# Kernel tuning notes

Measured on AMD Instinct MI355X. Metric: run time of the kernel, lower is better.

## Reference

```python
import jax, jax.numpy as jnp
import numpy as np

B, S, D_IN, D_H, D_OUT = 4, 2048, 512, 512, 512


def setup_inputs() -> dict:
    key = jax.random.key(0)
    ks = jax.random.split(key, 11)
    s_in = 1.0 / np.sqrt(D_IN)
    s_cat = 1.0 / np.sqrt(3 * D_H)
    return {
        "x1": jax.random.normal(ks[0], (B, S, D_IN), jnp.float32),
        "x2": jax.random.normal(ks[1], (B, S, D_IN), jnp.float32),
        "x3": jax.random.normal(ks[2], (B, S, D_IN), jnp.float32),
        "Wq": jax.random.normal(ks[3], (D_IN, D_H), jnp.float32) * s_in,
        "bq": jnp.zeros((D_H,), jnp.float32),
        "Wk": jax.random.normal(ks[4], (D_IN, D_H), jnp.float32) * s_in,
        "bk": jnp.zeros((D_H,), jnp.float32),
        "Wv": jax.random.normal(ks[5], (D_IN, D_H), jnp.float32) * s_in,
        "bv": jnp.zeros((D_H,), jnp.float32),
        "Wo": jax.random.normal(ks[6], (3 * D_H, D_OUT), jnp.float32) * s_cat,
        "bo": jnp.zeros((D_OUT,), jnp.float32),
    }


def _attn(Q, K, V):
    # Q: [B,S,H], K/V: [B,S,H] -> [B,S,H]
    scale = 1.0 / jnp.sqrt(jnp.asarray(K.shape[-1], Q.dtype))
    scores = jnp.einsum('bqh,bkh->bqk', Q, K) * scale
    w = jax.nn.softmax(scores, axis=-1)
    return jnp.einsum('bqk,bkh->bqh', w, V)


def reference(x1, x2, x3, Wq, bq, Wk, bk, Wv, bv, Wo, bo):
    Q1, Q2, Q3 = x1 @ Wq + bq, x2 @ Wq + bq, x3 @ Wq + bq
    K1, K2, K3 = x1 @ Wk + bk, x2 @ Wk + bk, x3 @ Wk + bk
    V1, V2, V3 = x1 @ Wv + bv, x2 @ Wv + bv, x3 @ Wv + bv
    fused_x1 = _attn(Q1, K2, V2) + _attn(Q1, K3, V3)
    fused_x2 = _attn(Q2, K1, V1) + _attn(Q2, K3, V3)
    fused_x3 = _attn(Q3, K1, V1) + _attn(Q3, K2, V2)
    fused = jnp.concatenate([fused_x1, fused_x2, fused_x3], axis=-1)
    return fused @ Wo + bo
```

## Files before the change

kernel.cpp:

```cpp
#include <hip/hip_runtime.h>
#include <hip/hip_bf16.h>

typedef __attribute__((ext_vector_type(4))) float  f32x4;
typedef __attribute__((ext_vector_type(8))) short  short8;

#define GAS(p) ((const __attribute__((address_space(1))) void*)(p))
#define LAS(p) ((__attribute__((address_space(3))) void*)(p))

__device__ inline short bf16_of(float f) {
    union { float f; unsigned u; } v; v.f = f;
    unsigned r = v.u + 0x7FFFu + ((v.u >> 16) & 1u);
    return (short)(r >> 16);
}

#define MFMA __builtin_amdgcn_mfma_f32_16x16x32_bf16

__device__ __forceinline__ void stage64(const short* A, long lda,
                                        const short* B, long ldb,
                                        short* As, short* Bs) {
    const int tid = threadIdx.x;
    const int w = tid >> 6, l = tid & 63;
    const int r = l >> 3;
    const int scol = ((l & 7) ^ r) * 8;
#pragma unroll
    for (int q = 0; q < 4; ++q) {
        const int rowb = q * 32 + w * 8;
        __builtin_amdgcn_global_load_lds(GAS(A + (long)(rowb + r) * lda + scol),
                                         LAS(As + rowb * 64), 16, 0, 0);
        __builtin_amdgcn_global_load_lds(GAS(B + (long)(rowb + r) * ldb + scol),
                                         LAS(Bs + rowb * 64), 16, 0, 0);
    }
}

__device__ __forceinline__ void gemm_core64(const short* A, long lda,
                                            const short* B, long ldb, int nk,
                                            short* sA, short* sB,
                                            f32x4 acc[4][4]) {
    const int tid = threadIdx.x;
    const int lane = tid & 63, wid = tid >> 6;
    const int wr = wid >> 1, wc = wid & 1;
    const int fr = lane & 15, fk = lane >> 4;
    const int swz = (fr & 7) << 4;
    const int abase = (wr * 64 + fr) * 128 + fk * 16;
    const int bbase = (wc * 64 + fr) * 128 + fk * 16;

    stage64(A, lda, B, ldb, sA, sB);
    __syncthreads();
    for (int ks = 0; ks < nk; ++ks) {
        const int cur = ks & 1;
        if (ks + 1 < nk)
            stage64(A + (ks + 1) * 64, lda, B + (ks + 1) * 64, ldb,
                    sA + (cur ^ 1) * 8192, sB + (cur ^ 1) * 8192);
        const char* pa = (const char*)(sA + cur * 8192);
        const char* pb = (const char*)(sB + cur * 8192);
        short8 af[2][4], bfr[2][4];
#pragma unroll
        for (int kk = 0; kk < 2; ++kk) {
#pragma unroll
            for (int mi = 0; mi < 4; ++mi)
                af[kk][mi] = *(const short8*)(pa + (((abase + kk * 64) ^ swz) + mi * 2048));
#pragma unroll
            for (int ni = 0; ni < 4; ++ni)
                bfr[kk][ni] = *(const short8*)(pb + (((bbase + kk * 64) ^ swz) + ni * 2048));
        }
#pragma unroll
        for (int kk = 0; kk < 2; ++kk)
#pragma unroll
            for (int mi = 0; mi < 4; ++mi)
#pragma unroll
                for (int ni = 0; ni < 4; ++ni)
                    acc[mi][ni] = MFMA(af[kk][mi], bfr[kk][ni], acc[mi][ni], 0, 0, 0);
        __syncthreads();
    }
}

__device__ __forceinline__ void bounce_store(short* Pb, const short vals[4][4][4],
                                             short* C, long ldc) {
    const int tid = threadIdx.x, lane = tid & 63, wid = tid >> 6;
    const int wr = wid >> 1, wc = wid & 1, fr = lane & 15, fk = lane >> 4;
#pragma unroll
    for (int mi = 0; mi < 4; ++mi)
#pragma unroll
        for (int ni = 0; ni < 4; ++ni)
#pragma unroll
            for (int r = 0; r < 4; ++r) {
                const int row = wr * 64 + mi * 16 + fk * 4 + r;
                const int col = wc * 64 + ni * 16 + fr;
                Pb[row * 128 + (col ^ ((row & 7) << 3))] = vals[mi][ni][r];
            }
    __syncthreads();
#pragma unroll
    for (int i = 0; i < 8; ++i) {
        const int row = i * 16 + (tid >> 4);
        const int ch = tid & 15;
        short8 v = *(const short8*)&Pb[row * 128 + ((ch * 8) ^ ((row & 7) << 3))];
        *(short8*)&C[(long)row * ldc + ch * 8] = v;
    }
}

__global__ __launch_bounds__(256, 2)
void proj_qk_k(const short* __restrict__ xb, const short* __restrict__ WqkT,
               short* __restrict__ Qb, short* __restrict__ Kb,
               const float* __restrict__ bq, const float* __restrict__ bk) {
    __shared__ short sA[2 * 8192], sB[2 * 8192];
    const short* Ab = xb + (long)blockIdx.x * 128 * 512;
    const short* Bb = WqkT + (long)blockIdx.y * 128 * 512;
    f32x4 acc[4][4] = {};
    gemm_core64(Ab, 512, Bb, 512, 8, sA, sB, acc);

    const int lane = threadIdx.x & 63, wid = threadIdx.x >> 6;
    const int wc = wid & 1, fr = lane & 15;
    const int qc0 = blockIdx.y * 128;
    const float* bias = qc0 < 512 ? bq + qc0 : bk + (qc0 - 512);
    short vals[4][4][4];
#pragma unroll
    for (int mi = 0; mi < 4; ++mi)
#pragma unroll
        for (int ni = 0; ni < 4; ++ni) {
            const float bv_ = bias[wc * 64 + ni * 16 + fr];
#pragma unroll
            for (int r = 0; r < 4; ++r)
                vals[mi][ni][r] = bf16_of(acc[mi][ni][r] + bv_);
        }
    short* dst = (qc0 < 512 ? Qb + qc0 : Kb + (qc0 - 512)) + (long)blockIdx.x * 128 * 512;
    bounce_store(sA, vals, dst, 512);
}

__global__ __launch_bounds__(256, 2)
void proj_vt_k(const short* __restrict__ WvT, const short* __restrict__ xb,
               short* __restrict__ VT, const float* __restrict__ bv) {
    __shared__ short sA[2 * 8192], sB[2 * 8192];
    const short* Ab = WvT + (long)blockIdx.x * 128 * 512;
    const short* Bb = xb + (long)blockIdx.y * 128 * 512;
    f32x4 acc[4][4] = {};
    gemm_core64(Ab, 512, Bb, 512, 8, sA, sB, acc);

    const int lane = threadIdx.x & 63, wid = threadIdx.x >> 6;
    const int wr = wid >> 1, fk = lane >> 4;
    short vals[4][4][4];
#pragma unroll
    for (int mi = 0; mi < 4; ++mi)
#pragma unroll
        for (int ni = 0; ni < 4; ++ni)
#pragma unroll
            for (int r = 0; r < 4; ++r) {
                const int rowg = blockIdx.x * 128 + wr * 64 + mi * 16 + fk * 4 + r;
                vals[mi][ni][r] = bf16_of(acc[mi][ni][r] + bv[rowg]);
            }
    bounce_store(sA, vals, VT + (long)blockIdx.x * 128 * 24576 + blockIdx.y * 128, 24576);
}

struct Off6 { long a[6], b[6]; };

__global__ __launch_bounds__(256, 2)
void qk_exp(const short* __restrict__ Qb, const short* __restrict__ Kb,
            short* __restrict__ Sc, float* __restrict__ lpart,
            Off6 o, int z0, int zmask, int zshift, float kscale) {
    __shared__ short sA[2 * 8192], sB[2 * 8192];
    const int bid = blockIdx.x;
    const int z = bid & zmask;
    const int t = bid >> zshift;
    const int bx = t & 15, by = t >> 4;
    const int slice = z0 + z;
    const int gp = slice >> 2, b = slice & 3;
    const short* Ab = Qb + o.a[gp] + ((long)b * 2048 + (long)bx * 128) * 512;
    const short* Bb = Kb + o.b[gp] + ((long)b * 2048 + (long)by * 128) * 512;
    f32x4 acc[4][4] = {};
    gemm_core64(Ab, 512, Bb, 512, 8, sA, sB, acc);

    const int tid = threadIdx.x, lane = tid & 63, wid = tid >> 6;
    const int wr = wid >> 1, wc = wid & 1, fr = lane & 15, fk = lane >> 4;

#pragma unroll
    for (int mi = 0; mi < 4; ++mi)
#pragma unroll
        for (int ni = 0; ni < 4; ++ni)
#pragma unroll
            for (int r = 0; r < 4; ++r)
                acc[mi][ni][r] = exp2f(acc[mi][ni][r] * kscale);

#pragma unroll
    for (int mi = 0; mi < 4; ++mi)
#pragma unroll
        for (int r = 0; r < 4; ++r) {
            float s = acc[mi][0][r] + acc[mi][1][r] + acc[mi][2][r] + acc[mi][3][r];
            s += __shfl_xor(s, 1); s += __shfl_xor(s, 2);
            s += __shfl_xor(s, 4); s += __shfl_xor(s, 8);
            if (fr == 0)
                lpart[((long)z * 32 + by * 2 + wc) * 2048 +
                      (long)bx * 128 + wr * 64 + mi * 16 + fk * 4 + r] = s;
        }

    short vals[4][4][4];
#pragma unroll
    for (int mi = 0; mi < 4; ++mi)
#pragma unroll
        for (int ni = 0; ni < 4; ++ni)
#pragma unroll
            for (int r = 0; r < 4; ++r)
                vals[mi][ni][r] = bf16_of(acc[mi][ni][r]);

    short* Cb = Sc + (long)z * 2048 * 2048 +
                (long)bx * 128 * 2048 + (long)by * 128;
    bounce_store(sA, vals, Cb, 2048);
}

struct POff { long v[6], c[6]; };

__global__ __launch_bounds__(256, 2)
void pv_div(const short* __restrict__ Sc, const short* __restrict__ VT,
            const float* __restrict__ lpart, short* __restrict__ F,
            POff o, int z0, int zmask, int zshift) {
    __shared__ short sA[2 * 8192], sB[2 * 8192];
    const int bid = blockIdx.x;
    const int z = bid & zmask;
    const int t = bid >> zshift;
    const int bx = t & 15, by = t >> 4;
    const int slice = z0 + z;
    const int gp = slice >> 2, b = slice & 3;
    const short* Ab = Sc + (long)z * 2048 * 2048 + (long)bx * 128 * 2048;
    const short* Bb = VT + o.v[gp] + (long)b * 2048 + (long)by * 128 * 24576;
    f32x4 acc[4][4] = {};
    gemm_core64(Ab, 2048, Bb, 24576, 32, sA, sB, acc);

    const int tid = threadIdx.x, lane = tid & 63, wid = tid >> 6;
    const int wr = wid >> 1, wc = wid & 1, fr = lane & 15, fk = lane >> 4;

    float* linv_s = (float*)sB;
    if (tid < 128) {
        const float* lp = lpart + ((long)z * 32) * 2048 + (long)bx * 128 + tid;
        float s = 0.f;
#pragma unroll
        for (int j = 0; j < 32; ++j) s += lp[(long)j * 2048];
        linv_s[tid] = 1.0f / s;
    }
    __syncthreads();

    short vals[4][4][4];
#pragma unroll
    for (int mi = 0; mi < 4; ++mi) {
        float linv[4];
#pragma unroll
        for (int r = 0; r < 4; ++r) linv[r] = linv_s[wr * 64 + mi * 16 + fk * 4 + r];
#pragma unroll
        for (int ni = 0; ni < 4; ++ni)
#pragma unroll
            for (int r = 0; r < 4; ++r)
                vals[mi][ni][r] = bf16_of(acc[mi][ni][r] * linv[r]);
    }
    __syncthreads();

    short* Cb = F + ((long)b * 2048 + (long)bx * 128) * 3072 +
                o.c[gp] + (long)by * 128;
    bounce_store(sA, vals, Cb, 3072);
}

__device__ __forceinline__ void stage_f(const short* A, const short* B,
                                        short* As, short* Bs) {
    const int tid = threadIdx.x, w = tid >> 6, l = tid & 63;
    const int r = l >> 3, scol = ((l & 7) ^ r) * 8;
#pragma unroll
    for (int q = 0; q < 4; ++q) {
        const int rowb = q * 32 + w * 8;
        __builtin_amdgcn_global_load_lds(GAS(A + (long)(rowb + r) * 3072 + scol),
                                         LAS(As + rowb * 64), 16, 0, 0);
    }
#pragma unroll
    for (int q = 0; q < 2; ++q) {
        const int rowb = q * 32 + w * 8;
        __builtin_amdgcn_global_load_lds(GAS(B + (long)(rowb + r) * 3072 + scol),
                                         LAS(Bs + rowb * 64), 16, 0, 0);
    }
}

__global__ __launch_bounds__(256, 3)
void final64(const short* __restrict__ A, const short* __restrict__ B,
             float* __restrict__ C, const float* __restrict__ bias) {
    __shared__ short sA[2 * 8192], sB[2 * 4096];
    const short* Ab = A + (long)blockIdx.x * 128 * 3072;
    const short* Bb = B + (long)blockIdx.y * 64 * 3072;
    const int tid = threadIdx.x, lane = tid & 63, w = tid >> 6;
    const int fr = lane & 15, fk = lane >> 4;
    const int swz = (fr & 7) << 4;
    const int abase = (w * 32 + fr) * 128 + fk * 16;
    const int bbase = fr * 128 + fk * 16;

    f32x4 acc[2][4] = {};
    stage_f(Ab, Bb, sA, sB);
    __syncthreads();
    for (int ks = 0; ks < 48; ++ks) {
        const int cur = ks & 1;
        if (ks + 1 < 48)
            stage_f(Ab + (ks + 1) * 64, Bb + (ks + 1) * 64,
                    sA + (cur ^ 1) * 8192, sB + (cur ^ 1) * 4096);
        const char* pa = (const char*)(sA + cur * 8192);
        const char* pb = (const char*)(sB + cur * 4096);
        short8 af[2][2], bf[2][4];
#pragma unroll
        for (int kk = 0; kk < 2; ++kk) {
#pragma unroll
            for (int mi = 0; mi < 2; ++mi)
                af[kk][mi] = *(const short8*)(pa + (((abase + kk * 64) ^ swz) + mi * 2048));
#pragma unroll
            for (int ni = 0; ni < 4; ++ni)
                bf[kk][ni] = *(const short8*)(pb + (((bbase + kk * 64) ^ swz) + ni * 2048));
        }
#pragma unroll
        for (int kk = 0; kk < 2; ++kk)
#pragma unroll
            for (int mi = 0; mi < 2; ++mi)
#pragma unroll
                for (int ni = 0; ni < 4; ++ni)
                    acc[mi][ni] = MFMA(af[kk][mi], bf[kk][ni], acc[mi][ni], 0, 0, 0);
        __syncthreads();
    }
    const long r0 = (long)blockIdx.x * 128 + w * 32 + fk * 4;
    const long c0 = (long)blockIdx.y * 64 + fr;
#pragma unroll
    for (int mi = 0; mi < 2; ++mi)
#pragma unroll
        for (int ni = 0; ni < 4; ++ni) {
            const long rr = r0 + mi * 16, cc = c0 + ni * 16;
#pragma unroll
            for (int r = 0; r < 4; ++r)
                C[(rr + r) * 512 + cc] = acc[mi][ni][r] + bias[cc];
        }
}

__global__ __launch_bounds__(256)
void xconv(const float* __restrict__ x0, const float* __restrict__ x1,
           const float* __restrict__ x2, short* __restrict__ xb) {
    const float* s = blockIdx.z == 0 ? x0 : (blockIdx.z == 1 ? x1 : x2);
    const long i = ((long)blockIdx.x * 256 + threadIdx.x) * 8;
    f32x4 a = *(const f32x4*)(s + i), c = *(const f32x4*)(s + i + 4);
    short8 v;
    v[0] = bf16_of(a.x); v[1] = bf16_of(a.y); v[2] = bf16_of(a.z); v[3] = bf16_of(a.w);
    v[4] = bf16_of(c.x); v[5] = bf16_of(c.y); v[6] = bf16_of(c.z); v[7] = bf16_of(c.w);
    *(short8*)(xb + (long)blockIdx.z * 8192 * 512 + i) = v;
}

__global__ __launch_bounds__(256)
void wprep(const float* __restrict__ Wq, const float* __restrict__ Wk,
           const float* __restrict__ Wv, const float* __restrict__ Wo,
           short* __restrict__ WqkT, short* __restrict__ WvT,
           short* __restrict__ WoT2) {
    __shared__ float t[32][33];
    const int z = blockIdx.z;
    const float* src; short* dst; int rows; long ldd; bool dup = false;
    if (z == 0)      { src = Wq; dst = WqkT;              rows = 512;  ldd = 512; }
    else if (z == 1) { src = Wk; dst = WqkT + 512L * 512; rows = 512;  ldd = 512; }
    else if (z == 2) { src = Wv; dst = WvT;               rows = 512;  ldd = 512; }
    else             { src = Wo; dst = WoT2;              rows = 1536; ldd = 3072; dup = true; }
    const int r0 = blockIdx.x * 32, c0 = blockIdx.y * 32;
    if (r0 >= rows) return;
    const int lx = threadIdx.x & 31, ly = threadIdx.x >> 5;
#pragma unroll
    for (int p = 0; p < 4; ++p)
        t[ly + 8 * p][lx] = src[(long)(r0 + ly + 8 * p) * 512 + (c0 + lx)];
    __syncthreads();
#pragma unroll
    for (int p = 0; p < 4; ++p) {
        const short v = bf16_of(t[lx][ly + 8 * p]);
        const long base = (long)(c0 + ly + 8 * p) * ldd + (r0 + lx);
        dst[base] = v;
        if (dup) dst[base + 1536] = v;
    }
}

extern "C" void kernel_launch(void* const* d_in, const int* in_sizes, int n_in,
                              void* d_out, int out_size, void* d_ws, size_t ws_size,
                              hipStream_t stream) {
    const float* x[3] = { (const float*)d_in[0], (const float*)d_in[1], (const float*)d_in[2] };
    const float* Wq = (const float*)d_in[3]; const float* bq = (const float*)d_in[4];
    const float* Wk = (const float*)d_in[5]; const float* bk = (const float*)d_in[6];
    const float* Wv = (const float*)d_in[7]; const float* bv = (const float*)d_in[8];
    const float* Wo = (const float*)d_in[9]; const float* bo = (const float*)d_in[10];

    const long TOK = 8192, T3 = 3 * TOK;

    char* ws = (char*)d_ws;
    size_t off = 0;
    auto alloc = [&](size_t bytes) -> void* {
        void* pp = ws + off;
        off += (bytes + 255) & ~(size_t)255;
        return pp;
    };

    short* WqkT  = (short*)alloc(1024L * 512 * 2);
    short* WvT   = (short*)alloc(512L * 512 * 2);
    short* WoT2  = (short*)alloc(512L * 3072 * 2);
    short* Qb    = (short*)alloc(T3 * 512 * 2);
    short* Kb    = (short*)alloc(T3 * 512 * 2);
    short* VT    = (short*)alloc(512L * T3 * 2);
    short* fused = (short*)alloc(TOK * 3072 * 2);
    float* lpart = (float*)alloc(8L * 32 * 2048 * 4);
    short* xb    = (short*)alloc(T3 * 512 * 2);

    const size_t SLICE = 2048L * 2048 * 2;
    const size_t rem = ws_size > off ? ws_size - off : 0;
    const int nsl = (rem >= 8 * SLICE) ? 8 : 4;
    const int zshift = (nsl == 8) ? 3 : 2;
    short* scores = (short*)alloc((size_t)nsl * SLICE);

    const dim3 tb(256);
    wprep<<<dim3(48, 16, 4), tb, 0, stream>>>(Wq, Wk, Wv, Wo, WqkT, WvT, WoT2);
    xconv<<<dim3(2048, 1, 3), tb, 0, stream>>>(x[0], x[1], x[2], xb);

    proj_qk_k<<<dim3(192, 8), tb, 0, stream>>>(xb, WqkT, Qb, Kb, bq, bk);
    proj_vt_k<<<dim3(4, 192), tb, 0, stream>>>(WvT, xb, VT, bv);

    const int imap[6] = {0, 1, 2, 0, 1, 2};
    const int jmap[6] = {1, 0, 0, 2, 2, 1};
    Off6 qo{}; POff po{};
    for (int gp = 0; gp < 6; ++gp) {
        qo.a[gp] = (long)imap[gp] * TOK * 512;
        qo.b[gp] = (long)jmap[gp] * TOK * 512;
        po.v[gp] = (long)jmap[gp] * TOK;
        po.c[gp] = (long)imap[gp] * 512 + (gp >= 3 ? 1536 : 0);
    }
    const float kscale = 0.04419417382415922f * 1.4426950408889634f;

    for (int z0 = 0; z0 < 24; z0 += nsl) {
        qk_exp<<<dim3(256 * nsl), tb, 0, stream>>>(Qb, Kb, scores, lpart, qo,
                                                   z0, nsl - 1, zshift, kscale);
        pv_div<<<dim3(64 * nsl), tb, 0, stream>>>(scores, VT, lpart, fused, po,
                                                  z0, nsl - 1, zshift);
    }

    final64<<<dim3(64, 8), tb, 0, stream>>>(fused, WoT2, (float*)d_out, bo);
}
```

Measured before the change: 415.4 us.

## Merge QK-exp and PV kernels into one launch with double-buffered score slices

Combines the score/exp kernel and the PV/normalize kernel into a single kernel that picks its role per block. When the workspace can hold 16 score slices, each launch runs the QK stage for chunk c alongside the PV stage for chunk c-1, using ping-pong score and lpart buffers and interleaving 4 QK blocks per PV block. The aim is to fill the GPU better and cut the tail idle time between dependent launches. In exchange it doubles the score and lpart workspace and adds a branch per block. If the workspace is too small, the code falls back to the old sequential schedule.

Result: no change. 419.4 us (+1.0%).

```diff
diff --git a/kernel.cpp b/kernel.cpp
--- a/kernel.cpp
+++ b/kernel.cpp
@@ -151,108 +151,106 @@
 }
 
 struct Off6 { long a[6], b[6]; };
+struct POff { long v[6], c[6]; };
 
 __global__ __launch_bounds__(256, 2)
-void qk_exp(const short* __restrict__ Qb, const short* __restrict__ Kb,
-            short* __restrict__ Sc, float* __restrict__ lpart,
-            Off6 o, int z0, int zmask, int zshift, float kscale) {
+void qkpv(const short* __restrict__ Qb, const short* __restrict__ Kb,
+          const short* __restrict__ VT,
+          short* __restrict__ ScQ, const short* __restrict__ ScP,
+          float* __restrict__ lpQ, const float* __restrict__ lpP,
+          short* __restrict__ F, Off6 qo, POff po,
+          int z0q, int z0p, int nqk, int npv,
+          int zmask, int zshift, float kscale) {
     __shared__ short sA[2 * 8192], sB[2 * 8192];
     const int bid = blockIdx.x;
-    const int z = bid & zmask;
-    const int t = bid >> zshift;
-    const int bx = t & 15, by = t >> 4;
-    const int slice = z0 + z;
-    const int gp = slice >> 2, b = slice & 3;
-    const short* Ab = Qb + o.a[gp] + ((long)b * 2048 + (long)bx * 128) * 512;
-    const short* Bb = Kb + o.b[gp] + ((long)b * 2048 + (long)by * 128) * 512;
-    f32x4 acc[4][4] = {};
-    gemm_core64(Ab, 512, Bb, 512, 8, sA, sB, acc);
-
+    bool isPv; int t;
+    if (nqk == 0)      { isPv = true;  t = bid; }
+    else if (npv == 0) { isPv = false; t = bid; }
+    else {
+        const int q5 = bid / 5, r5 = bid - q5 * 5;
+        isPv = (r5 == 4);
+        t = isPv ? q5 : q5 * 4 + r5;
+    }
     const int tid = threadIdx.x, lane = tid & 63, wid = tid >> 6;
     const int wr = wid >> 1, wc = wid & 1, fr = lane & 15, fk = lane >> 4;
-
-#pragma unroll
-    for (int mi = 0; mi < 4; ++mi)
-#pragma unroll
-        for (int ni = 0; ni < 4; ++ni)
-#pragma unroll
-            for (int r = 0; r < 4; ++r)
-                acc[mi][ni][r] = exp2f(acc[mi][ni][r] * kscale);
-
-#pragma unroll
-    for (int mi = 0; mi < 4; ++mi)
-#pragma unroll
-        for (int r = 0; r < 4; ++r) {
-            float s = acc[mi][0][r] + acc[mi][1][r] + acc[mi][2][r] + acc[mi][3][r];
-            s += __shfl_xor(s, 1); s += __shfl_xor(s, 2);
-            s += __shfl_xor(s, 4); s += __shfl_xor(s, 8);
-            if (fr == 0)
-                lpart[((long)z * 32 + by * 2 + wc) * 2048 +
-                      (long)bx * 128 + wr * 64 + mi * 16 + fk * 4 + r] = s;
-        }
-
-    short vals[4][4][4];
-#pragma unroll
-    for (int mi = 0; mi < 4; ++mi)
-#pragma unroll
-        for (int ni = 0; ni < 4; ++ni)
-#pragma unroll
-            for (int r = 0; r < 4; ++r)
-                vals[mi][ni][r] = bf16_of(acc[mi][ni][r]);
-
-    short* Cb = Sc + (long)z * 2048 * 2048 +
-                (long)bx * 128 * 2048 + (long)by * 128;
-    bounce_store(sA, vals, Cb, 2048);
-}
-
-struct POff { long v[6], c[6]; };
-
-__global__ __launch_bounds__(256, 2)
-void pv_div(const short* __restrict__ Sc, const short* __restrict__ VT,
-            const float* __restrict__ lpart, short* __restrict__ F,
-            POff o, int z0, int zmask, int zshift) {
-    __shared__ short sA[2 * 8192], sB[2 * 8192];
-    const int bid = blockIdx.x;
-    const int z = bid & zmask;
-    const int t = bid >> zshift;
-    const int bx = t & 15, by = t >> 4;
-    const int slice = z0 + z;
-    const int gp = slice >> 2, b = slice & 3;
-    const short* Ab = Sc + (long)z * 2048 * 2048 + (long)bx * 128 * 2048;
-    const short* Bb = VT + o.v[gp] + (long)b * 2048 + (long)by * 128 * 24576;
-    f32x4 acc[4][4] = {};
-    gemm_core64(Ab, 2048, Bb, 24576, 32, sA, sB, acc);
-
-    const int tid = threadIdx.x, lane = tid & 63, wid = tid >> 6;
-    const int wr = wid >> 1, wc = wid & 1, fr = lane & 15, fk = lane >> 4;
-
-    float* linv_s = (float*)sB;
-    if (tid < 128) {
-        const float* lp = lpart + ((long)z * 32) * 2048 + (long)bx * 128 + tid;
-        float s = 0.f;
-#pragma unroll
-        for (int j = 0; j < 32; ++j) s += lp[(long)j * 2048];
-        linv_s[tid] = 1.0f / s;
-    }
-    __syncthreads();
-
-    short vals[4][4][4];
-#pragma unroll
-    for (int mi = 0; mi < 4; ++mi) {
-        float linv[4];
-#pragma unroll
-        for (int r = 0; r < 4; ++r) linv[r] = linv_s[wr * 64 + mi * 16 + fk * 4 + r];
-#pragma unroll
-        for (int ni = 0; ni < 4; ++ni)
-#pragma unroll
-            for (int r = 0; r < 4; ++r)
-                vals[mi][ni][r] = bf16_of(acc[mi][ni][r] * linv[r]);
-    }
-    __syncthreads();
-
-    short* Cb = F + ((long)b * 2048 + (long)bx * 128) * 3072 +
-                o.c[gp] + (long)by * 128;
-    bounce_store(sA, vals, Cb, 3072);
+    const int z = t & zmask;
+    const int tt = t >> zshift;
+    const int bx = tt & 15, by = tt >> 4;
+
+    if (!isPv) {
+        const int slice = z0q + z, gp = slice >> 2, b = slice & 3;
+        const short* Ab = Qb + qo.a[gp] + ((long)b * 2048 + (long)bx * 128) * 512;
+        const short* Bb = Kb + qo.b[gp] + ((long)b * 2048 + (long)by * 128) * 512;
+        f32x4 acc[4][4] = {};
+        gemm_core64(Ab, 512, Bb, 512, 8, sA, sB, acc);
+
+#pragma unroll
+        for (int mi = 0; mi < 4; ++mi)
+#pragma unroll
+            for (int ni = 0; ni < 4; ++ni)
+#pragma unroll
+                for (int r = 0; r < 4; ++r)
+                    acc[mi][ni][r] = exp2f(acc[mi][ni][r] * kscale);
+
+#pragma unroll
+        for (int mi = 0; mi < 4; ++mi)
+#pragma unroll
+            for (int r = 0; r < 4; ++r) {
+                float s = acc[mi][0][r] + acc[mi][1][r] + acc[mi][2][r] + acc[mi][3][r];
+                s += __shfl_xor(s, 1); s += __shfl_xor(s, 2);
+                s += __shfl_xor(s, 4); s += __shfl_xor(s, 8);
+                if (fr == 0)
+                    lpQ[((long)z * 32 + by * 2 + wc) * 2048 +
+                        (long)bx * 128 + wr * 64 + mi * 16 + fk * 4 + r] = s;
+            }
+
+        short vals[4][4][4];
+#pragma unroll
+        for (int mi = 0; mi < 4; ++mi)
+#pragma unroll
+            for (int ni = 0; ni < 4; ++ni)
+#pragma unroll
+                for (int r = 0; r < 4; ++r)
+                    vals[mi][ni][r] = bf16_of(acc[mi][ni][r]);
+
+        short* Cb = ScQ + (long)z * 2048 * 2048 +
+                    (long)bx * 128 * 2048 + (long)by * 128;
+        bounce_store(sA, vals, Cb, 2048);
+    } else {
+        const int slice = z0p + z, gp = slice >> 2, b = slice & 3;
+        const short* Ab = ScP + (long)z * 2048 * 2048 + (long)bx * 128 * 2048;
+        const short* Bb = VT + po.v[gp] + (long)b * 2048 + (long)by * 128 * 24576;
+        f32x4 acc[4][4] = {};
+        gemm_core64(Ab, 2048, Bb, 24576, 32, sA, sB, acc);
+
+        float* linv_s = (float*)sB;
+        if (tid < 128) {
+            const float* lp = lpP + ((long)z * 32) * 2048 + (long)bx * 128 + tid;
+            float s = 0.f;
+#pragma unroll
+            for (int j = 0; j < 32; ++j) s += lp[(long)j * 2048];
+            linv_s[tid] = 1.0f / s;
+        }
+        __syncthreads();
+
+        short vals[4][4][4];
+#pragma unroll
+        for (int mi = 0; mi < 4; ++mi) {
+            float linv[4];
+#pragma unroll
+            for (int r = 0; r < 4; ++r) linv[r] = linv_s[wr * 64 + mi * 16 + fk * 4 + r];
+#pragma unroll
+            for (int ni = 0; ni < 4; ++ni)
+#pragma unroll
+                for (int r = 0; r < 4; ++r)
+                    vals[mi][ni][r] = bf16_of(acc[mi][ni][r] * linv[r]);
+        }
+        __syncthreads();
+
+        short* Cb = F + ((long)b * 2048 + (long)bx * 128) * 3072 +
+                    po.c[gp] + (long)by * 128;
+        bounce_store(sA, vals, Cb, 3072);
+    }
 }
 
 __device__ __forceinline__ void stage_f(const short* A, const short* B,
@@ -393,14 +391,16 @@
     short* Kb    = (short*)alloc(T3 * 512 * 2);
     short* VT    = (short*)alloc(512L * T3 * 2);
     short* fused = (short*)alloc(TOK * 3072 * 2);
-    float* lpart = (float*)alloc(8L * 32 * 2048 * 4);
+    float* lpart = (float*)alloc(16L * 32 * 2048 * 4);
     short* xb    = (short*)alloc(T3 * 512 * 2);
 
     const size_t SLICE = 2048L * 2048 * 2;
     const size_t rem = ws_size > off ? ws_size - off : 0;
-    const int nsl = (rem >= 8 * SLICE) ? 8 : 4;
-    const int zshift = (nsl == 8) ? 3 : 2;
-    short* scores = (short*)alloc((size_t)nsl * SLICE);
+    int tier;
+    if      (rem >= 16 * SLICE) tier = 2;
+    else if (rem >=  8 * SLICE) tier = 1;
+    else                        tier = 0;
+    short* scores = (short*)alloc((tier == 2 ? 16 : (tier == 1 ? 8 : 4)) * SLICE);
 
     const dim3 tb(256);
     wprep<<<dim3(48, 16, 4), tb, 0, stream>>>(Wq, Wk, Wv, Wo, WqkT, WvT, WoT2);
@@ -419,12 +419,33 @@
         po.c[gp] = (long)imap[gp] * 512 + (gp >= 3 ? 1536 : 0);
     }
     const float kscale = 0.04419417382415922f * 1.4426950408889634f;
-
-    for (int z0 = 0; z0 < 24; z0 += nsl) {
-        qk_exp<<<dim3(256 * nsl), tb, 0, stream>>>(Qb, Kb, scores, lpart, qo,
-                                                   z0, nsl - 1, zshift, kscale);
-        pv_div<<<dim3(64 * nsl), tb, 0, stream>>>(scores, VT, lpart, fused, po,
-                                                  z0, nsl - 1, zshift);
+    const long SL8 = 8L * 2048 * 2048;
+    const long LP8 = 8L * 32 * 2048;
+
+    if (tier == 2) {
+        for (int c = 0; c < 4; ++c) {
+            const int nqk = (c < 3) ? 2048 : 0;
+            const int npv = (c > 0) ? 512 : 0;
+            qkpv<<<dim3(nqk + npv), tb, 0, stream>>>(
+                Qb, Kb, VT,
+                scores + (size_t)(c & 1) * SL8, scores + (size_t)((c + 1) & 1) * SL8,
+                lpart + (size_t)(c & 1) * LP8, lpart + (size_t)((c + 1) & 1) * LP8,
+                fused, qo, po, c * 8, (c - 1) * 8, nqk, npv, 7, 3, kscale);
+        }
+    } else if (tier == 1) {
+        for (int z0 = 0; z0 < 24; z0 += 8) {
+            qkpv<<<dim3(2048), tb, 0, stream>>>(Qb, Kb, VT, scores, scores,
+                lpart, lpart, fused, qo, po, z0, 0, 2048, 0, 7, 3, kscale);
+            qkpv<<<dim3(512), tb, 0, stream>>>(Qb, Kb, VT, scores, scores,
+                lpart, lpart, fused, qo, po, 0, z0, 0, 512, 7, 3, kscale);
+        }
+    } else {
+        for (int z0 = 0; z0 < 24; z0 += 4) {
+            qkpv<<<dim3(1024), tb, 0, stream>>>(Qb, Kb, VT, scores, scores,
+                lpart, lpart, fused, qo, po, z0, 0, 1024, 0, 3, 2, kscale);
+            qkpv<<<dim3(256), tb, 0, stream>>>(Qb, Kb, VT, scores, scores,
+                lpart, lpart, fused, qo, po, 0, z0, 0, 256, 3, 2, kscale);
+        }
     }
 
     final64<<<dim3(64, 8), tb, 0, stream>>>(fused, WoT2, (float*)d_out, bo);
```

## Give qk_exp its own BK=32 double-buffered GEMM loop at higher occupancy

Applied to the files above, without the earlier changes.

Replaces the shared gemm_core64 call in qk_exp with an inline main loop of K-step 32. It uses a single 32KB LDS buffer, double-buffered through global_load_lds with an XOR swizzle, and has one barrier per step. The launch bound rises from 2 to 4 blocks per CU, so more waves can hide load latency in the Q·K^T stage. The trade-off is twice as many barriers and K iterations, plus tighter register limits that could cause spills.

Measured after the change: 401.0 us, median of 3. 1.04x faster.

```diff
diff --git a/kernel.cpp b/kernel.cpp
--- a/kernel.cpp
+++ b/kernel.cpp
@@ -152,24 +152,67 @@
 
 struct Off6 { long a[6], b[6]; };
 
-__global__ __launch_bounds__(256, 2)
+__global__ __launch_bounds__(256, 4)
 void qk_exp(const short* __restrict__ Qb, const short* __restrict__ Kb,
             short* __restrict__ Sc, float* __restrict__ lpart,
             Off6 o, int z0, int zmask, int zshift, float kscale) {
-    __shared__ short sA[2 * 8192], sB[2 * 8192];
+    __shared__ short lds[16384];
+    short* As = lds;
+    short* Bs = lds + 8192;
     const int bid = blockIdx.x;
     const int z = bid & zmask;
     const int t = bid >> zshift;
     const int bx = t & 15, by = t >> 4;
     const int slice = z0 + z;
     const int gp = slice >> 2, b = slice & 3;
-    const short* Ab = Qb + o.a[gp] + ((long)b * 2048 + (long)bx * 128) * 512;
-    const short* Bb = Kb + o.b[gp] + ((long)b * 2048 + (long)by * 128) * 512;
-    f32x4 acc[4][4] = {};
-    gemm_core64(Ab, 512, Bb, 512, 8, sA, sB, acc);
+    const short* A = Qb + o.a[gp] + ((long)b * 2048 + (long)bx * 128) * 512;
+    const short* B = Kb + o.b[gp] + ((long)b * 2048 + (long)by * 128) * 512;
 
     const int tid = threadIdx.x, lane = tid & 63, wid = tid >> 6;
     const int wr = wid >> 1, wc = wid & 1, fr = lane & 15, fk = lane >> 4;
+    const int sr = tid >> 2;
+    const int scc = (((tid & 3) ^ (sr & 3)) * 8);
+    const int arow = wr * 64 + fr, brow = wc * 64 + fr;
+
+    auto stage = [&](const short* Ap, const short* Bp, int cur) {
+        short* ad = As + cur * 4096;
+        short* bd = Bs + cur * 4096;
+        __builtin_amdgcn_global_load_lds(GAS(Ap + (long)sr * 512 + scc),
+                                         LAS(ad + sr * 32 + (tid & 3) * 8), 16, 0, 0);
+        __builtin_amdgcn_global_load_lds(GAS(Ap + (long)(sr + 64) * 512 + scc),
+                                         LAS(ad + (sr + 64) * 32 + (tid & 3) * 8), 16, 0, 0);
+        __builtin_amdgcn_global_load_lds(GAS(Bp + (long)sr * 512 + scc),
+                                         LAS(bd + sr * 32 + (tid & 3) * 8), 16, 0, 0);
+        __builtin_amdgcn_global_load_lds(GAS(Bp + (long)(sr + 64) * 512 + scc),
+                                         LAS(bd + (sr + 64) * 32 + (tid & 3) * 8), 16, 0, 0);
+    };
+
+    f32x4 acc[4][4] = {};
+    stage(A, B, 0);
+    __syncthreads();
+    for (int ks = 0; ks < 16; ++ks) {
+        const int cur = ks & 1;
+        if (ks + 1 < 16) stage(A + (ks + 1) * 32, B + (ks + 1) * 32, cur ^ 1);
+        const short* pa = As + cur * 4096;
+        const short* pb = Bs + cur * 4096;
+        short8 af[4], bf[4];
+#pragma unroll
+        for (int mi = 0; mi < 4; ++mi) {
+            const int row = arow + mi * 16;
+            af[mi] = *(const short8*)&pa[row * 32 + ((fk ^ (row & 3)) * 8)];
+        }
+#pragma unroll
+        for (int ni = 0; ni < 4; ++ni) {
+            const int row = brow + ni * 16;
+            bf[ni] = *(const short8*)&pb[row * 32 + ((fk ^ (row & 3)) * 8)];
+        }
+#pragma unroll
+        for (int mi = 0; mi < 4; ++mi)
+#pragma unroll
+            for (int ni = 0; ni < 4; ++ni)
+                acc[mi][ni] = MFMA(af[mi], bf[ni], acc[mi][ni], 0, 0, 0);
+        __syncthreads();
+    }
 
 #pragma unroll
     for (int mi = 0; mi < 4; ++mi)
@@ -202,7 +245,7 @@
 
     short* Cb = Sc + (long)z * 2048 * 2048 +
                 (long)bx * 128 * 2048 + (long)by * 128;
-    bounce_store(sA, vals, Cb, 2048);
+    bounce_store(lds, vals, Cb, 2048);
 }
 
 struct POff { long v[6], c[6]; };
```
